# Kernel tuning notes

Measured on AMD Instinct MI355X. Metric: run time of the kernel, lower is better.

The kernel has to match this reference:

```python
import jax, jax.numpy as jnp
import numpy as np

B, N, C, H = 2, 2048, 1024, 16
D = C // H  # head_dim = 64


def _rope_freqs(n, d_half, theta=10000.0):
    inv = 1.0 / (theta ** (np.arange(0, d_half, dtype=np.float32) / d_half))
    ang = np.arange(n, dtype=np.float32)[:, None] * inv[None, :]
    return jnp.asarray(np.cos(ang)), jnp.asarray(np.sin(ang))


def setup_inputs() -> dict:
    key = jax.random.key(0)
    ks = jax.random.split(key, 5)
    cos, sin = _rope_freqs(N, D // 2)
    s = 0.02
    return {
        "x": jax.random.normal(ks[0], (B, N, C), jnp.float32),
        "w_qkv": jax.random.normal(ks[1], (3 * C, C), jnp.float32) * s,
        "b_qkv": jnp.zeros((3 * C,), jnp.float32),
        "w_proj": jax.random.normal(ks[2], (C, C), jnp.float32) * s,
        "b_proj": jnp.zeros((C,), jnp.float32),
        "freqs_cos": cos,
        "freqs_sin": sin,
    }


def _apply_rope(t, cos, sin):
    # t: (B, H, N, D); consecutive pairs (even, odd) form complex numbers,
    # matching torch.view_as_complex on reshape(..., D//2, 2).
    te = t[..., 0::2]
    to = t[..., 1::2]
    cos = cos[None, None, :, :]  # (1,1,N,D//2)
    sin = sin[None, None, :, :]
    oe = te * cos - to * sin
    oo = te * sin + to * cos
    return jnp.stack([oe, oo], axis=-1).reshape(t.shape)


def reference(x, w_qkv, b_qkv, w_proj, b_proj, freqs_cos, freqs_sin):
    b, n, c = x.shape
    qkv = x @ w_qkv.T + b_qkv                      # (B,N,3C)
    qkv = qkv.reshape(b, n, 3, H, D).transpose(2, 0, 3, 1, 4)  # (3,B,H,N,D)
    q, k, v = qkv[0], qkv[1], qkv[2]
    q = _apply_rope(q, freqs_cos, freqs_sin)
    k = _apply_rope(k, freqs_cos, freqs_sin)
    scale = 1.0 / jnp.sqrt(jnp.asarray(D, x.dtype))
    scores = jnp.einsum("bhqd,bhkd->bhqk", q, k) * scale
    attn = jax.nn.softmax(scores, axis=-1)
    out = jnp.einsum("bhqk,bhkd->bhqd", attn, v)   # (B,H,N,D)
    out = out.transpose(0, 2, 1, 3).reshape(b, n, c)
    return out @ w_proj.T + b_proj
```

## Files before the change

kernel.cpp:

```cpp
#include <hip/hip_runtime.h>
#include <hip/hip_bf16.h>
#include <stdint.h>

#define BB 2
#define NN 2048
#define CC 1024
#define HH 16
#define DD 64
#define C3 3072

typedef __attribute__((ext_vector_type(8))) short bf16x8;
typedef __attribute__((ext_vector_type(4))) float f32x4;
typedef __attribute__((ext_vector_type(4))) unsigned short ushort4_t;
typedef __attribute__((ext_vector_type(2))) unsigned short ushort2_t;

__device__ __forceinline__ unsigned short f2bf(float f) {
  union { float f; unsigned u; } v; v.f = f;
  unsigned r = v.u + 0x7FFFu + ((v.u >> 16) & 1u);
  return (unsigned short)(r >> 16);
}

#define GLDS(g, l) __builtin_amdgcn_global_load_lds( \
    (const __attribute__((address_space(1))) void*)(g), \
    (__attribute__((address_space(3))) void*)(l), 16, 0, 0)

__global__ __launch_bounds__(256) void k_f32_to_bf16(
    const float* __restrict__ s, unsigned short* __restrict__ d, int n4)
{
  int i = blockIdx.x * 256 + threadIdx.x;
  if (i >= n4) return;
  float4 v = ((const float4*)s)[i];
  ushort4_t o;
  o.x = f2bf(v.x); o.y = f2bf(v.y); o.z = f2bf(v.z); o.w = f2bf(v.w);
  ((ushort4_t*)d)[i] = o;
}

__global__ __launch_bounds__(256) void k_gemm_bt_bias(
    const unsigned short* __restrict__ A, const unsigned short* __restrict__ Bt,
    const float* __restrict__ bias, float* __restrict__ Co,
    int M, int Nn, int K)
{
  __shared__ __align__(16) unsigned short As[128 * 32];
  __shared__ __align__(16) unsigned short Bs[128 * 32];
  const int tid  = threadIdx.x;
  const int lane = tid & 63;
  const int wave = tid >> 6;
  const int bm = blockIdx.y * 128;
  const int bn = blockIdx.x * 128;
  const int wm = (wave >> 1) * 64;
  const int wn = (wave & 1) * 64;
  const int frow = lane & 15;
  const int fk   = (lane >> 4) * 8;

  f32x4 acc[4][4] = {};

  const int row0 = tid >> 2, cc0 = tid & 3;
  const int row1 = row0 + 64;

  for (int k0 = 0; k0 < K; k0 += 32) {
    GLDS(A  + (size_t)(bm + row0) * K + k0 + cc0 * 8, As + (size_t)tid * 8);
    GLDS(Bt + (size_t)(bn + row0) * K + k0 + cc0 * 8, Bs + (size_t)tid * 8);
    GLDS(A  + (size_t)(bm + row1) * K + k0 + cc0 * 8, As + (size_t)(tid + 256) * 8);
    GLDS(Bt + (size_t)(bn + row1) * K + k0 + cc0 * 8, Bs + (size_t)(tid + 256) * 8);
    __syncthreads();

    bf16x8 af[4], bfr[4];
#pragma unroll
    for (int t = 0; t < 4; ++t) {
      af[t]  = *(const bf16x8*)(As + (wm + t * 16 + frow) * 32 + fk);
      bfr[t] = *(const bf16x8*)(Bs + (wn + t * 16 + frow) * 32 + fk);
    }
#pragma unroll
    for (int mt = 0; mt < 4; ++mt)
#pragma unroll
      for (int nt = 0; nt < 4; ++nt)
        acc[mt][nt] = __builtin_amdgcn_mfma_f32_16x16x32_bf16(af[mt], bfr[nt], acc[mt][nt], 0, 0, 0);
    __syncthreads();
  }

  const int er0  = (lane >> 4) * 4;
  const int ecol = lane & 15;
#pragma unroll
  for (int nt = 0; nt < 4; ++nt) {
    int col = bn + wn + nt * 16 + ecol;
    float bv = bias[col];
#pragma unroll
    for (int mt = 0; mt < 4; ++mt)
#pragma unroll
      for (int r = 0; r < 4; ++r) {
        int rowg = bm + wm + mt * 16 + er0 + r;
        Co[(size_t)rowg * Nn + col] = acc[mt][nt][r] + bv;
      }
  }
}

__global__ __launch_bounds__(256) void k_pack_qk(
    const float* __restrict__ qkv, const float* __restrict__ cosb,
    const float* __restrict__ sinb,
    unsigned short* __restrict__ Qg, unsigned short* __restrict__ Kg)
{
  int t = blockIdx.x * 256 + threadIdx.x;
  int i = t & 31;
  int n = (t >> 5) & (NN - 1);
  int h = (t >> 16) & (HH - 1);
  int b = t >> 20;
  const float* base = qkv + (size_t)(b * NN + n) * C3 + h * DD;
  float2 qv = *(const float2*)(base + 2 * i);
  float2 kv = *(const float2*)(base + CC + 2 * i);
  float c = cosb[n * 32 + i], s = sinb[n * 32 + i];
  size_t o = ((size_t)((b * HH + h) * NN + n)) * DD + 2 * i;
  ushort2_t qo, ko;
  qo.x = f2bf((qv.x * c - qv.y * s) * 0.125f);
  qo.y = f2bf((qv.x * s + qv.y * c) * 0.125f);
  ko.x = f2bf(kv.x * c - kv.y * s);
  ko.y = f2bf(kv.x * s + kv.y * c);
  *(ushort2_t*)(Qg + o) = qo;
  *(ushort2_t*)(Kg + o) = ko;
}

__global__ __launch_bounds__(256) void k_pack_v(
    const float* __restrict__ qkv, unsigned short* __restrict__ Vtg)
{
  __shared__ float tile[64][65];
  int bh = blockIdx.x >> 5;
  int n0 = (blockIdx.x & 31) * 64;
  int b = bh >> 4, h = bh & 15;
  int tx = threadIdx.x & 63;
  int ty = threadIdx.x >> 6;
  const float* src = qkv + (size_t)(b * NN + n0) * C3 + 2 * CC + h * DD;
#pragma unroll
  for (int i2 = 0; i2 < 16; ++i2) {
    int nl = i2 * 4 + ty;
    tile[nl][tx] = src[(size_t)nl * C3 + tx];
  }
  __syncthreads();
  unsigned short* dst = Vtg + (size_t)bh * DD * NN + n0;
#pragma unroll
  for (int i2 = 0; i2 < 16; ++i2) {
    int d = i2 * 4 + ty;
    dst[(size_t)d * NN + tx] = f2bf(tile[tx][d]);
  }
}

__global__ __launch_bounds__(256) void k_attn(
    const unsigned short* __restrict__ Qg, const unsigned short* __restrict__ Kg,
    const unsigned short* __restrict__ Vtg, unsigned short* __restrict__ Og)
{
  __shared__ __align__(16) unsigned short Ks[2][64 * 64];
  __shared__ __align__(16) unsigned short Vs[2][64 * 64];
  __shared__ __align__(16) unsigned short Ps[4][16 * 64];

  const int tid  = threadIdx.x;
  const int lane = tid & 63;
  const int wave = tid >> 6;
  const int bh = blockIdx.x >> 5;
  const int qt = blockIdx.x & 31;
  const int q0 = qt * 64 + wave * 16;
  const int frow   = lane & 15;
  const int fchunk = lane >> 4;
  const int er0  = (lane >> 4) * 4;
  const int ecol = lane & 15;

  const unsigned short* Qb = Qg  + (size_t)bh * NN * DD;
  const unsigned short* Kb = Kg  + (size_t)bh * NN * DD;
  const unsigned short* Vb = Vtg + (size_t)bh * DD * NN;

  bf16x8 qf[2];
#pragma unroll
  for (int kt = 0; kt < 2; ++kt)
    qf[kt] = *(const bf16x8*)(Qb + (size_t)(q0 + frow) * DD + kt * 32 + fchunk * 8);

  bf16x8 ones;
#pragma unroll
  for (int i = 0; i < 8; ++i) ones[i] = (short)0x3F80;

  f32x4 oacc[4] = {};
  f32x4 lacc = {};

  const int row0 = tid >> 3, cc0 = tid & 7;
  const int sw0 = (cc0 ^ (row0 & 7)) * 8;

  GLDS(Kb + (size_t)row0 * DD + sw0,        Ks[0] + (size_t)tid * 8);
  GLDS(Vb + (size_t)row0 * NN + sw0,        Vs[0] + (size_t)tid * 8);
  GLDS(Kb + (size_t)(row0 + 32) * DD + sw0, Ks[0] + (size_t)(tid + 256) * 8);
  GLDS(Vb + (size_t)(row0 + 32) * NN + sw0, Vs[0] + (size_t)(tid + 256) * 8);

  for (int t = 0; t < NN / 64; ++t) {
    const int p = t & 1;
    __syncthreads();

    if (t + 1 < NN / 64) {
      const int j = (t + 1) * 64;
      GLDS(Kb + (size_t)(j + row0) * DD + sw0,      Ks[1 - p] + (size_t)tid * 8);
      GLDS(Vb + (size_t)row0 * NN + j + sw0,        Vs[1 - p] + (size_t)tid * 8);
      GLDS(Kb + (size_t)(j + row0 + 32) * DD + sw0, Ks[1 - p] + (size_t)(tid + 256) * 8);
      GLDS(Vb + (size_t)(row0 + 32) * NN + j + sw0, Vs[1 - p] + (size_t)(tid + 256) * 8);
    }

    f32x4 sacc[4] = {};
#pragma unroll
    for (int nt = 0; nt < 4; ++nt) {
      int kr = nt * 16 + frow;
      bf16x8 kf0 = *(const bf16x8*)(Ks[p] + kr * 64 + ((fchunk       ^ (kr & 7)) << 3));
      bf16x8 kf1 = *(const bf16x8*)(Ks[p] + kr * 64 + (((fchunk + 4) ^ (kr & 7)) << 3));
      sacc[nt] = __builtin_amdgcn_mfma_f32_16x16x32_bf16(qf[0], kf0, sacc[nt], 0, 0, 0);
      sacc[nt] = __builtin_amdgcn_mfma_f32_16x16x32_bf16(qf[1], kf1, sacc[nt], 0, 0, 0);
    }

#pragma unroll
    for (int r = 0; r < 4; ++r) {
      int prow = er0 + r;
#pragma unroll
      for (int nt = 0; nt < 4; ++nt) {
        float pv = __expf(sacc[nt][r]);
        int col = nt * 16 + ecol;
        Ps[wave][prow * 64 + (((col >> 3) ^ (prow & 7)) << 3) + (col & 7)] = f2bf(pv);
      }
    }

    bf16x8 pf0 = *(const bf16x8*)(&Ps[wave][frow * 64 + ((fchunk       ^ (frow & 7)) << 3)]);
    bf16x8 pf1 = *(const bf16x8*)(&Ps[wave][frow * 64 + (((fchunk + 4) ^ (frow & 7)) << 3)]);
    lacc = __builtin_amdgcn_mfma_f32_16x16x32_bf16(pf0, ones, lacc, 0, 0, 0);
    lacc = __builtin_amdgcn_mfma_f32_16x16x32_bf16(pf1, ones, lacc, 0, 0, 0);
#pragma unroll
    for (int dt = 0; dt < 4; ++dt) {
      int vr = dt * 16 + frow;
      bf16x8 vf0 = *(const bf16x8*)(Vs[p] + vr * 64 + ((fchunk       ^ (vr & 7)) << 3));
      bf16x8 vf1 = *(const bf16x8*)(Vs[p] + vr * 64 + (((fchunk + 4) ^ (vr & 7)) << 3));
      oacc[dt] = __builtin_amdgcn_mfma_f32_16x16x32_bf16(pf0, vf0, oacc[dt], 0, 0, 0);
      oacc[dt] = __builtin_amdgcn_mfma_f32_16x16x32_bf16(pf1, vf1, oacc[dt], 0, 0, 0);
    }
  }

  const int b = bh >> 4;
  const int h = bh & 15;
#pragma unroll
  for (int dt = 0; dt < 4; ++dt) {
#pragma unroll
    for (int r = 0; r < 4; ++r) {
      int qrow = q0 + er0 + r;
      int d = dt * 16 + ecol;
      float v = oacc[dt][r] / lacc[r];
      Og[(size_t)(b * NN + qrow) * CC + h * DD + d] = f2bf(v);
    }
  }
}

extern "C" void kernel_launch(void* const* d_in, const int* in_sizes, int n_in,
                              void* d_out, int out_size, void* d_ws, size_t ws_size,
                              hipStream_t stream)
{
  const float* x      = (const float*)d_in[0];
  const float* w_qkv  = (const float*)d_in[1];
  const float* b_qkv  = (const float*)d_in[2];
  const float* w_proj = (const float*)d_in[3];
  const float* b_proj = (const float*)d_in[4];
  const float* fcos   = (const float*)d_in[5];
  const float* fsin   = (const float*)d_in[6];
  float* out = (float*)d_out;

  char* ws = (char*)d_ws;
  unsigned short* xb     = (unsigned short*)(ws);
  unsigned short* wqkvb  = (unsigned short*)(ws + 8388608);
  unsigned short* wprojb = (unsigned short*)(ws + 14680064);
  float*          qkvf   = (float*)(ws + 16777216);
  unsigned short* Qb     = (unsigned short*)(ws + 67108864);
  unsigned short* Kb     = (unsigned short*)(ws + 75497472);
  unsigned short* Vtb    = (unsigned short*)(ws + 83886080);
  unsigned short* aob    = (unsigned short*)(ws + 92274688);

  k_f32_to_bf16<<<4096, 256, 0, stream>>>(x, xb, 1048576);
  k_f32_to_bf16<<<3072, 256, 0, stream>>>(w_qkv, wqkvb, 786432);
  k_f32_to_bf16<<<1024, 256, 0, stream>>>(w_proj, wprojb, 262144);

  k_gemm_bt_bias<<<dim3(24, 32), 256, 0, stream>>>(xb, wqkvb, b_qkv, qkvf,
                                                   4096, 3072, 1024);
  k_pack_qk<<<8192, 256, 0, stream>>>(qkvf, fcos, fsin, Qb, Kb);
  k_pack_v<<<1024, 256, 0, stream>>>(qkvf, Vtb);

  k_attn<<<1024, 256, 0, stream>>>(Qb, Kb, Vtb, aob);

  k_gemm_bt_bias<<<dim3(8, 32), 256, 0, stream>>>(aob, wprojb, b_proj, out,
                                                  4096, 1024, 1024);
}
```

Measured before the change: 231.8 us.

## Fuse RoPE/QKV packing into GEMM epilogue, merge conversions, use exp2 in attention

The QKV GEMM epilogue now applies bias, RoPE (partner element via lane shuffle), and Q scaling, and writes bf16 Q/K/V directly. This removes the fp32 qkv intermediate and the separate pack kernels, and a small bf16 transpose kernel produces V^T. The three conversion launches become one, and softmax uses exp2 with log2e folded into the Q scale plus truncating bf16 conversion. The projection GEMM uses 64-row tiles so more blocks run. The epilogue stores are scattered 2-byte writes, and truncation changes rounding slightly.

```diff
diff --git a/kernel.cpp b/kernel.cpp
--- a/kernel.cpp
+++ b/kernel.cpp
@@ -12,7 +12,6 @@
 typedef __attribute__((ext_vector_type(8))) short bf16x8;
 typedef __attribute__((ext_vector_type(4))) float f32x4;
 typedef __attribute__((ext_vector_type(4))) unsigned short ushort4_t;
-typedef __attribute__((ext_vector_type(2))) unsigned short ushort2_t;
 
 __device__ __forceinline__ unsigned short f2bf(float f) {
   union { float f; unsigned u; } v; v.f = f;
@@ -20,25 +19,41 @@
   return (unsigned short)(r >> 16);
 }
 
+#if __has_builtin(__builtin_amdgcn_exp2f)
+#define EXP2(x) __builtin_amdgcn_exp2f(x)
+#else
+#define EXP2(x) exp2f(x)
+#endif
+
+#define QSCALE 0.18033688f
+
 #define GLDS(g, l) __builtin_amdgcn_global_load_lds( \
     (const __attribute__((address_space(1))) void*)(g), \
     (__attribute__((address_space(3))) void*)(l), 16, 0, 0)
 
-__global__ __launch_bounds__(256) void k_f32_to_bf16(
-    const float* __restrict__ s, unsigned short* __restrict__ d, int n4)
-{
-  int i = blockIdx.x * 256 + threadIdx.x;
-  if (i >= n4) return;
+__global__ __launch_bounds__(256) void k_cvt(
+    const float* __restrict__ x, const float* __restrict__ wq,
+    const float* __restrict__ wp,
+    unsigned short* __restrict__ xb, unsigned short* __restrict__ wqb,
+    unsigned short* __restrict__ wpb)
+{
+  int blk = blockIdx.x;
+  const float* s; unsigned short* d; int i;
+  if (blk < 4096)      { s = x;  d = xb;  i = blk * 256 + threadIdx.x; }
+  else if (blk < 7168) { s = wq; d = wqb; i = (blk - 4096) * 256 + threadIdx.x; }
+  else                 { s = wp; d = wpb; i = (blk - 7168) * 256 + threadIdx.x; }
   float4 v = ((const float4*)s)[i];
   ushort4_t o;
   o.x = f2bf(v.x); o.y = f2bf(v.y); o.z = f2bf(v.z); o.w = f2bf(v.w);
   ((ushort4_t*)d)[i] = o;
 }
 
-__global__ __launch_bounds__(256) void k_gemm_bt_bias(
+__global__ __launch_bounds__(256) void k_gemm_qkv(
     const unsigned short* __restrict__ A, const unsigned short* __restrict__ Bt,
-    const float* __restrict__ bias, float* __restrict__ Co,
-    int M, int Nn, int K)
+    const float* __restrict__ bias,
+    const float* __restrict__ cosb, const float* __restrict__ sinb,
+    unsigned short* __restrict__ Qg, unsigned short* __restrict__ Kg,
+    unsigned short* __restrict__ Vnd)
 {
   __shared__ __align__(16) unsigned short As[128 * 32];
   __shared__ __align__(16) unsigned short Bs[128 * 32];
@@ -51,6 +66,7 @@
   const int wn = (wave & 1) * 64;
   const int frow = lane & 15;
   const int fk   = (lane >> 4) * 8;
+  const int K = 1024;
 
   f32x4 acc[4][4] = {};
 
@@ -80,65 +96,67 @@
 
   const int er0  = (lane >> 4) * 4;
   const int ecol = lane & 15;
+  const int region = bn >> 10;
+  unsigned short* dstQK = (region == 0) ? Qg : Kg;
+
 #pragma unroll
   for (int nt = 0; nt < 4; ++nt) {
-    int col = bn + wn + nt * 16 + ecol;
-    float bv = bias[col];
+    const int col = bn + wn + nt * 16 + ecol;
+    const float bv = bias[col];
+    const int c64 = (wn + nt * 16 + ecol) & 63;
+    const int h   = (col >> 6) & 15;
+    const int ii  = c64 >> 1;
 #pragma unroll
     for (int mt = 0; mt < 4; ++mt)
 #pragma unroll
       for (int r = 0; r < 4; ++r) {
-        int rowg = bm + wm + mt * 16 + er0 + r;
-        Co[(size_t)rowg * Nn + col] = acc[mt][nt][r] + bv;
+        const int rowg = bm + wm + mt * 16 + er0 + r;
+        const int b = rowg >> 11, n = rowg & (NN - 1);
+        float v = acc[mt][nt][r] + bv;
+        float vp = __shfl_xor(v, 1, 64);
+        const size_t o = ((size_t)(b * HH + h) * NN + n) * DD + c64;
+        if (region == 2) {
+          Vnd[o] = f2bf(v);
+        } else {
+          float cth = cosb[n * 32 + ii], sth = sinb[n * 32 + ii];
+          float ov = (c64 & 1) ? (vp * sth + v * cth)
+                               : (v * cth - vp * sth);
+          if (region == 0) ov *= QSCALE;
+          dstQK[o] = f2bf(ov);
+        }
       }
   }
 }
 
-__global__ __launch_bounds__(256) void k_pack_qk(
-    const float* __restrict__ qkv, const float* __restrict__ cosb,
-    const float* __restrict__ sinb,
-    unsigned short* __restrict__ Qg, unsigned short* __restrict__ Kg)
-{
-  int t = blockIdx.x * 256 + threadIdx.x;
-  int i = t & 31;
-  int n = (t >> 5) & (NN - 1);
-  int h = (t >> 16) & (HH - 1);
-  int b = t >> 20;
-  const float* base = qkv + (size_t)(b * NN + n) * C3 + h * DD;
-  float2 qv = *(const float2*)(base + 2 * i);
-  float2 kv = *(const float2*)(base + CC + 2 * i);
-  float c = cosb[n * 32 + i], s = sinb[n * 32 + i];
-  size_t o = ((size_t)((b * HH + h) * NN + n)) * DD + 2 * i;
-  ushort2_t qo, ko;
-  qo.x = f2bf((qv.x * c - qv.y * s) * 0.125f);
-  qo.y = f2bf((qv.x * s + qv.y * c) * 0.125f);
-  ko.x = f2bf(kv.x * c - kv.y * s);
-  ko.y = f2bf(kv.x * s + kv.y * c);
-  *(ushort2_t*)(Qg + o) = qo;
-  *(ushort2_t*)(Kg + o) = ko;
-}
-
-__global__ __launch_bounds__(256) void k_pack_v(
-    const float* __restrict__ qkv, unsigned short* __restrict__ Vtg)
-{
-  __shared__ float tile[64][65];
-  int bh = blockIdx.x >> 5;
-  int n0 = (blockIdx.x & 31) * 64;
-  int b = bh >> 4, h = bh & 15;
-  int tx = threadIdx.x & 63;
-  int ty = threadIdx.x >> 6;
-  const float* src = qkv + (size_t)(b * NN + n0) * C3 + 2 * CC + h * DD;
-#pragma unroll
-  for (int i2 = 0; i2 < 16; ++i2) {
-    int nl = i2 * 4 + ty;
-    tile[nl][tx] = src[(size_t)nl * C3 + tx];
+__global__ __launch_bounds__(256) void k_vt(
+    const unsigned short* __restrict__ Vnd, unsigned short* __restrict__ Vt)
+{
+  __shared__ unsigned short t[64][66];
+  const int tid = threadIdx.x;
+  const int bh = blockIdx.x >> 5;
+  const int n0 = (blockIdx.x & 31) * 64;
+
+  const unsigned short* src = Vnd + ((size_t)bh * NN + n0) * DD;
+  const int nl = tid >> 2, d0 = (tid & 3) * 16;
+#pragma unroll
+  for (int j = 0; j < 4; ++j) {
+    ushort4_t v = *(const ushort4_t*)(src + (size_t)nl * DD + d0 + j * 4);
+    t[nl][d0 + j * 4 + 0] = v.x;
+    t[nl][d0 + j * 4 + 1] = v.y;
+    t[nl][d0 + j * 4 + 2] = v.z;
+    t[nl][d0 + j * 4 + 3] = v.w;
   }
   __syncthreads();
-  unsigned short* dst = Vtg + (size_t)bh * DD * NN + n0;
-#pragma unroll
-  for (int i2 = 0; i2 < 16; ++i2) {
-    int d = i2 * 4 + ty;
-    dst[(size_t)d * NN + tx] = f2bf(tile[tx][d]);
+  const int d = tid >> 2, m0 = (tid & 3) * 16;
+  unsigned short* dst = Vt + ((size_t)bh * DD + d) * NN + n0 + m0;
+#pragma unroll
+  for (int j = 0; j < 4; ++j) {
+    ushort4_t o;
+    o.x = t[m0 + j * 4 + 0][d];
+    o.y = t[m0 + j * 4 + 1][d];
+    o.z = t[m0 + j * 4 + 2][d];
+    o.w = t[m0 + j * 4 + 3][d];
+    *(ushort4_t*)(dst + j * 4) = o;
   }
 }
 
@@ -212,9 +230,11 @@
       int prow = er0 + r;
 #pragma unroll
       for (int nt = 0; nt < 4; ++nt) {
-        float pv = __expf(sacc[nt][r]);
+        float pv = EXP2(sacc[nt][r]);
+        union { float f; unsigned u; } cv; cv.f = pv;
         int col = nt * 16 + ecol;
-        Ps[wave][prow * 64 + (((col >> 3) ^ (prow & 7)) << 3) + (col & 7)] = f2bf(pv);
+        Ps[wave][prow * 64 + (((col >> 3) ^ (prow & 7)) << 3) + (col & 7)] =
+            (unsigned short)(cv.u >> 16);
       }
     }
 
@@ -243,6 +263,64 @@
       float v = oacc[dt][r] / lacc[r];
       Og[(size_t)(b * NN + qrow) * CC + h * DD + d] = f2bf(v);
     }
+  }
+}
+
+__global__ __launch_bounds__(256) void k_gemm_proj(
+    const unsigned short* __restrict__ A, const unsigned short* __restrict__ Bt,
+    const float* __restrict__ bias, float* __restrict__ Co)
+{
+  __shared__ __align__(16) unsigned short As[64 * 32];
+  __shared__ __align__(16) unsigned short Bs[128 * 32];
+  const int tid  = threadIdx.x;
+  const int lane = tid & 63;
+  const int wave = tid >> 6;
+  const int bm = blockIdx.y * 64;
+  const int bn = blockIdx.x * 128;
+  const int wm = (wave >> 1) * 32;
+  const int wn = (wave & 1) * 64;
+  const int frow = lane & 15;
+  const int fk   = (lane >> 4) * 8;
+  const int K = 1024;
+
+  f32x4 acc[2][4] = {};
+
+  const int row0 = tid >> 2, cc0 = tid & 3;
+
+  for (int k0 = 0; k0 < K; k0 += 32) {
+    GLDS(A  + (size_t)(bm + row0) * K + k0 + cc0 * 8, As + (size_t)tid * 8);
+    GLDS(Bt + (size_t)(bn + row0) * K + k0 + cc0 * 8, Bs + (size_t)tid * 8);
+    GLDS(Bt + (size_t)(bn + row0 + 64) * K + k0 + cc0 * 8, Bs + (size_t)(tid + 256) * 8);
+    __syncthreads();
+
+    bf16x8 af[2], bfr[4];
+#pragma unroll
+    for (int t = 0; t < 2; ++t)
+      af[t] = *(const bf16x8*)(As + (wm + t * 16 + frow) * 32 + fk);
+#pragma unroll
+    for (int t = 0; t < 4; ++t)
+      bfr[t] = *(const bf16x8*)(Bs + (wn + t * 16 + frow) * 32 + fk);
+#pragma unroll
+    for (int mt = 0; mt < 2; ++mt)
+#pragma unroll
+      for (int nt = 0; nt < 4; ++nt)
+        acc[mt][nt] = __builtin_amdgcn_mfma_f32_16x16x32_bf16(af[mt], bfr[nt], acc[mt][nt], 0, 0, 0);
+    __syncthreads();
+  }
+
+  const int er0  = (lane >> 4) * 4;
+  const int ecol = lane & 15;
+#pragma unroll
+  for (int nt = 0; nt < 4; ++nt) {
+    int col = bn + wn + nt * 16 + ecol;
+    float bv = bias[col];
+#pragma unroll
+    for (int mt = 0; mt < 2; ++mt)
+#pragma unroll
+      for (int r = 0; r < 4; ++r) {
+        int rowg = bm + wm + mt * 16 + er0 + r;
+        Co[(size_t)rowg * CC + col] = acc[mt][nt][r] + bv;
+      }
   }
 }
 
@@ -263,23 +341,19 @@
   unsigned short* xb     = (unsigned short*)(ws);
   unsigned short* wqkvb  = (unsigned short*)(ws + 8388608);
   unsigned short* wprojb = (unsigned short*)(ws + 14680064);
-  float*          qkvf   = (float*)(ws + 16777216);
-  unsigned short* Qb     = (unsigned short*)(ws + 67108864);
-  unsigned short* Kb     = (unsigned short*)(ws + 75497472);
-  unsigned short* Vtb    = (unsigned short*)(ws + 83886080);
-  unsigned short* aob    = (unsigned short*)(ws + 92274688);
-
-  k_f32_to_bf16<<<4096, 256, 0, stream>>>(x, xb, 1048576);
-  k_f32_to_bf16<<<3072, 256, 0, stream>>>(w_qkv, wqkvb, 786432);
-  k_f32_to_bf16<<<1024, 256, 0, stream>>>(w_proj, wprojb, 262144);
-
-  k_gemm_bt_bias<<<dim3(24, 32), 256, 0, stream>>>(xb, wqkvb, b_qkv, qkvf,
-                                                   4096, 3072, 1024);
-  k_pack_qk<<<8192, 256, 0, stream>>>(qkvf, fcos, fsin, Qb, Kb);
-  k_pack_v<<<1024, 256, 0, stream>>>(qkvf, Vtb);
+  unsigned short* Qb     = (unsigned short*)(ws + 16777216);
+  unsigned short* Kb     = (unsigned short*)(ws + 25165824);
+  unsigned short* Vnd    = (unsigned short*)(ws + 33554432);
+  unsigned short* Vtb    = (unsigned short*)(ws + 41943040);
+  unsigned short* aob    = (unsigned short*)(ws + 50331648);
+
+  k_cvt<<<8192, 256, 0, stream>>>(x, w_qkv, w_proj, xb, wqkvb, wprojb);
+
+  k_gemm_qkv<<<dim3(24, 32), 256, 0, stream>>>(xb, wqkvb, b_qkv, fcos, fsin,
+                                               Qb, Kb, Vnd);
+  k_vt<<<1024, 256, 0, stream>>>(Vnd, Vtb);
 
   k_attn<<<1024, 256, 0, stream>>>(Qb, Kb, Vtb, aob);
 
-  k_gemm_bt_bias<<<dim3(8, 32), 256, 0, stream>>>(aob, wprojb, b_proj, out,
-                                                  4096, 1024, 1024);
-}
+  k_gemm_proj<<<dim3(8, 64), 256, 0, stream>>>(aob, wprojb, b_proj, out);
+}
```

New measurement: 218.8 us. 1.06x faster.
